# Optimization experiments

Hardware: AMD Instinct MI355X
Metric: run time of the kernel (lower is better)

The kernel has to match this reference:

```python
import jax, jax.numpy as jnp
import numpy as np

D = 512            # token_dim * num_heads
TOKEN_DIM = 256
SCALE = TOKEN_DIM ** (-0.5)
EPS = 1e-12        # torch F.normalize eps
FIDX = (0, 1, 1)   # original bug: out_rv uses final_myo


def l2norm(x, axis):
    n = jnp.sqrt(jnp.sum(x * x, axis=axis, keepdims=True))
    return x / jnp.maximum(n, EPS)


def setup_inputs() -> dict:
    key = jax.random.key(0)
    ks = jax.random.split(key, 16)
    B, N = 16, 1024
    s = 0.02
    return {
        "x_lv": jax.random.normal(ks[0], (B, N, D), jnp.float32),
        "x_myo": jax.random.normal(ks[1], (B, N, D), jnp.float32),
        "x_rv": jax.random.normal(ks[2], (B, N, D), jnp.float32),
        # stacked per-branch params: branch 0=lv, 1=myo, 2=rv
        "Wq": jax.random.normal(ks[3], (3, D, D), jnp.float32) * s,
        "bq": jax.random.normal(ks[4], (3, D), jnp.float32) * s,
        "Wk": jax.random.normal(ks[5], (3, D, D), jnp.float32) * s,
        "bk": jax.random.normal(ks[6], (3, D), jnp.float32) * s,
        "wg": jax.random.normal(ks[7], (3, D, 1), jnp.float32),
        "Wp": jax.random.normal(ks[8], (3, 3, D, D), jnp.float32) * s,  # [branch, key_src]
        "bp": jax.random.normal(ks[9], (3, 3, D), jnp.float32) * s,
        "Wf": jax.random.normal(ks[10], (3, D, TOKEN_DIM), jnp.float32) * s,
        "bf": jax.random.normal(ks[11], (3, TOKEN_DIM), jnp.float32) * s,
    }


def reference(x_lv, x_myo, x_rv, Wq, bq, Wk, bk, wg, Wp, bp, Wf, bf):
    X = (x_lv, x_myo, x_rv)
    # projections + L2 normalize over feature dim
    Q = [l2norm(X[m] @ Wq[m] + bq[m], axis=-1) for m in range(3)]  # [B,N,D]
    K = [l2norm(X[m] @ Wk[m] + bk[m], axis=-1) for m in range(3)]  # [B,N,D]
    outs = []
    for m in range(3):
        A = l2norm((Q[m] @ wg[m]) * SCALE, axis=1)       # [B,N,1], normed over seq
        G = jnp.sum(A * Q[m], axis=1)[:, None, :]        # [B,1,D] (broadcast repeat)
        acc = Q[m]
        for j in range(3):
            acc = acc + (G * K[j]) @ Wp[m, j] + bp[m, j]
        outs.append(acc @ Wf[FIDX[m]] + bf[FIDX[m]])     # [B,N,token_dim]
    return tuple(outs)
```

## Files before the change

kernel.cpp:

```cpp
#include <hip/hip_runtime.h>
#include <hip/hip_bf16.h>

typedef __hip_bfloat16 bf16;
typedef __attribute__((ext_vector_type(8))) short short8;
typedef __attribute__((ext_vector_type(4))) float f32x4;

#define SCALE_F 0.0625f

__device__ __forceinline__ float b2f(short s) {
  union { float f; unsigned int u; } x;
  x.u = ((unsigned int)(unsigned short)s) << 16;
  return x.f;
}
__device__ __forceinline__ unsigned short f2bu(float f) {
  __hip_bfloat16 h = __float2bfloat16(f);
  unsigned short u;
  __builtin_memcpy(&u, &h, 2);
  return u;
}
__device__ __forceinline__ void store_out(float* p, float v) { *p = v; }
__device__ __forceinline__ void store_out(bf16* p, float v) { *p = __float2bfloat16(v); }

typedef __attribute__((address_space(3))) void lds_void;
typedef __attribute__((address_space(1))) void gbl_void;

__device__ __forceinline__ void lds_load16(void* l, const void* g) {
  __builtin_amdgcn_global_load_lds((const gbl_void*)g, (lds_void*)l, 16, 0, 0);
}

template<typename OutT>
__device__ __forceinline__ void gemm_tile(
    const bf16* A0, const bf16* A1, const bf16* A2, const bf16* A3,
    int ldA, const bf16* Bt, int ldB, OutT* C, int ldC,
    const float* bias, int K, int row0, int col0)
{
  __shared__ bf16 As[128 * 32];
  __shared__ bf16 Bs[128 * 32];
  const int t = threadIdx.x;
  const int lane = t & 63;
  const int w = t >> 6;
  const int wm = w >> 1, wn = w & 1;
  const int lr = lane & 15, hi = lane >> 4;
  const int rA = t >> 2;
  const int kA = (t & 3) * 8;

  f32x4 acc[4][4];
#pragma unroll
  for (int i = 0; i < 4; ++i)
#pragma unroll
    for (int j = 0; j < 4; ++j) acc[i][j] = (f32x4){0.f, 0.f, 0.f, 0.f};

  const int nk = K >> 5;
  for (int kt = 0; kt < nk; ++kt) {
    const int k0 = kt << 5;
    const int s = k0 >> 9;
    const bf16* Aseg = (s == 0) ? A0 : (s == 1) ? A1 : (s == 2) ? A2 : A3;
    const int kl = (k0 & 511) + kA;
    __syncthreads();
    lds_load16(&As[t * 8],        Aseg + (size_t)(row0 + rA) * ldA + kl);
    lds_load16(&As[2048 + t * 8], Aseg + (size_t)(row0 + 64 + rA) * ldA + kl);
    lds_load16(&Bs[t * 8],        Bt + (size_t)(col0 + rA) * ldB + k0 + kA);
    lds_load16(&Bs[2048 + t * 8], Bt + (size_t)(col0 + 64 + rA) * ldB + k0 + kA);
    __syncthreads();
    short8 af[4], bfr[4];
#pragma unroll
    for (int f = 0; f < 4; ++f)
      af[f] = *(const short8*)&As[(wm * 64 + f * 16 + lr) * 32 + hi * 8];
#pragma unroll
    for (int f = 0; f < 4; ++f)
      bfr[f] = *(const short8*)&Bs[(wn * 64 + f * 16 + lr) * 32 + hi * 8];
#pragma unroll
    for (int i = 0; i < 4; ++i)
#pragma unroll
      for (int j = 0; j < 4; ++j)
        acc[i][j] = __builtin_amdgcn_mfma_f32_16x16x32_bf16(af[i], bfr[j], acc[i][j], 0, 0, 0);
  }

#pragma unroll
  for (int i = 0; i < 4; ++i) {
    const int rowb = row0 + wm * 64 + i * 16 + hi * 4;
#pragma unroll
    for (int j = 0; j < 4; ++j) {
      const int col = col0 + wn * 64 + j * 16 + lr;
      const float bv = bias ? bias[col] : 0.f;
      f32x4 v = acc[i][j];
#pragma unroll
      for (int r = 0; r < 4; ++r)
        store_out(&C[(size_t)(rowb + r) * ldC + col], v[r] + bv);
    }
  }
}

__global__ __launch_bounds__(256) void k_convert_x(
    const float* __restrict__ x0, const float* __restrict__ x1,
    const float* __restrict__ x2, bf16* __restrict__ xbf)
{
  const long long i = (long long)blockIdx.x * 256 + threadIdx.x;
  const int tt = (int)(i / 2097152);
  const long long e = i - (long long)tt * 2097152;
  const float4* src = (const float4*)(tt == 0 ? x0 : tt == 1 ? x1 : x2);
  float4 v = src[e];
  ushort4 o;
  o.x = f2bu(v.x); o.y = f2bu(v.y); o.z = f2bu(v.z); o.w = f2bu(v.w);
  ((ushort4*)xbf)[i] = o;
}

__global__ __launch_bounds__(256) void k_transpose(
    const float* __restrict__ in, bf16* __restrict__ out, int R, int C)
{
  const int tilesC = C >> 6;
  const int tr = (blockIdx.x / tilesC) << 6;
  const int tc = (blockIdx.x % tilesC) << 6;
  const size_t base = (size_t)blockIdx.y * R * C;
  __shared__ unsigned short tile[64][72];
  const int rr = threadIdx.x >> 4;
  const int cc = (threadIdx.x & 15) << 2;
#pragma unroll
  for (int p = 0; p < 4; ++p) {
    const int r = rr + (p << 4);
    float4 v = *(const float4*)&in[base + (size_t)(tr + r) * C + tc + cc];
    tile[cc + 0][r] = f2bu(v.x);
    tile[cc + 1][r] = f2bu(v.y);
    tile[cc + 2][r] = f2bu(v.z);
    tile[cc + 3][r] = f2bu(v.w);
  }
  __syncthreads();
#pragma unroll
  for (int p = 0; p < 4; ++p) {
    const int r = rr + (p << 4);
    ushort4 o;
    o.x = tile[r][cc + 0];
    o.y = tile[r][cc + 1];
    o.z = tile[r][cc + 2];
    o.w = tile[r][cc + 3];
    *(ushort4*)&out[base + (size_t)(tc + r) * R + tr + cc] = o;
  }
}

__global__ __launch_bounds__(256) void k_copy_bf16(
    const float* __restrict__ in, bf16* __restrict__ out)
{
  const long long i = (long long)blockIdx.x * 256 + threadIdx.x;
  float4 v = ((const float4*)in)[i];
  ushort4 o;
  o.x = f2bu(v.x); o.y = f2bu(v.y); o.z = f2bu(v.z); o.w = f2bu(v.w);
  ((ushort4*)out)[i] = o;
}

__global__ __launch_bounds__(256) void k_bprime(
    const float* __restrict__ bp, const float* __restrict__ Wf,
    const float* __restrict__ bfv, float* __restrict__ bpr)
{
  const int m = blockIdx.x;
  const int dc = blockIdx.y;
  const int n = threadIdx.x;
  const int fi = (m == 0) ? 0 : 1;
  float s = (dc == 0) ? bfv[fi * 256 + n] : 0.f;
  for (int d = dc * 64; d < dc * 64 + 64; ++d) {
    float b3 = bp[(m * 3 + 0) * 512 + d] + bp[(m * 3 + 1) * 512 + d] +
               bp[(m * 3 + 2) * 512 + d];
    s += b3 * Wf[(size_t)fi * 512 * 256 + (size_t)d * 256 + n];
  }
  atomicAdd(&bpr[m * 256 + n], s);
}

__global__ __launch_bounds__(256) void k_gemm1(
    const bf16* __restrict__ Xbf, const bf16* __restrict__ WT,
    const float* __restrict__ bq, const float* __restrict__ bk,
    bf16* __restrict__ QK)
{
  const int bid = blockIdx.x;
  const int swz = (bid & 7) * 384 + (bid >> 3);
  const int inst = swz >> 9;
  const int bx = swz & 511;
  const int m = (inst >= 3) ? inst - 3 : inst;
  const int tm = bx >> 2, tn = bx & 3;
  const bf16* A = Xbf + (size_t)m * (16384 * 512);
  const bf16* B = WT + (size_t)inst * (512 * 512);
  const float* bias = (inst < 3 ? bq : bk) + m * 512;
  bf16* C = QK + (size_t)inst * (16384 * 512);
  gemm_tile<bf16>(A, A, A, A, 512, B, 512, C, 512, bias, 512, tm * 128, tn * 128);
}

__global__ __launch_bounds__(256) void k_gemm_wpf(
    const bf16* __restrict__ WfT, const bf16* __restrict__ Wpbf,
    float* __restrict__ WpfT)
{
  const int inst = blockIdx.y;
  const int m = inst / 3;
  const int fi = (m == 0) ? 0 : 1;
  const int tm = blockIdx.x >> 2, tn = blockIdx.x & 3;
  const bf16* A = WfT + (size_t)fi * (256 * 512);
  const bf16* B = Wpbf + (size_t)inst * (512 * 512);
  float* C = WpfT + (size_t)inst * (256 * 512);
  gemm_tile<float>(A, A, A, A, 512, B, 512, C, 512, nullptr, 512, tm * 128, tn * 128);
}

__global__ __launch_bounds__(256) void k_gemm2(
    const bf16* __restrict__ QK, const bf16* __restrict__ W2T,
    const float* __restrict__ bpr, float* __restrict__ out)
{
  const int bid = blockIdx.x;
  const int swz = (bid & 7) * 96 + (bid >> 3);
  const int e = swz >> 4;
  const int bx = swz & 15;
  const int m = e >> 4, b = e & 15;
  const int tm = bx >> 1, tn = bx & 1;
  const bf16* A0 = QK + ((size_t)m * 16384 + (size_t)b * 1024) * 512;
  const bf16* A1 = QK + ((size_t)(3 * 16384) + (size_t)b * 1024) * 512;
  const bf16* A2 = QK + ((size_t)(4 * 16384) + (size_t)b * 1024) * 512;
  const bf16* A3 = QK + ((size_t)(5 * 16384) + (size_t)b * 1024) * 512;
  const bf16* Bt = W2T + (size_t)e * (256 * 2048);
  float* C = out + (size_t)e * (1024 * 256);
  gemm_tile<float>(A0, A1, A2, A3, 512, Bt, 2048, C, 256, bpr + m * 256, 2048,
                   tm * 128, tn * 128);
}

__global__ __launch_bounds__(256) void k_norm(
    bf16* __restrict__ QK, const float* __restrict__ wg, float* __restrict__ qdot)
{
  const int row = blockIdx.x * 4 + (threadIdx.x >> 6);
  const int lane = threadIdx.x & 63;
  bf16* p = QK + (size_t)row * 512 + lane * 8;
  short8 v = *(const short8*)p;
  float f[8];
  float ss = 0.f;
#pragma unroll
  for (int i = 0; i < 8; ++i) { f[i] = b2f(v[i]); ss += f[i] * f[i]; }
#pragma unroll
  for (int o = 32; o; o >>= 1) ss += __shfl_xor(ss, o);
  const float inv = 1.f / fmaxf(sqrtf(ss), 1e-12f);
  short8 ov;
#pragma unroll
  for (int i = 0; i < 8; ++i) ov[i] = (short)f2bu(f[i] * inv);
  *(short8*)p = ov;
  const int tt = row >> 14;
  if (tt < 3) {
    const float* wgm = wg + (size_t)tt * 512 + lane * 8;
    float dot = 0.f;
#pragma unroll
    for (int i = 0; i < 8; ++i) dot += f[i] * wgm[i];
    dot *= inv;
#pragma unroll
    for (int o = 32; o; o >>= 1) dot += __shfl_xor(dot, o);
    if (lane == 0) qdot[row] = dot;
  }
}

__global__ __launch_bounds__(256) void k_G(
    const float* __restrict__ qdot, const bf16* __restrict__ QK, float* __restrict__ G)
{
  const int e = blockIdx.x;
  const int m = e >> 4, b = e & 15;
  const int d0 = blockIdx.y << 6;
  __shared__ float Al[1024];
  __shared__ float red[4];
  __shared__ float Gp[4][64];
  const int t = threadIdx.x;
  const float* qd = qdot + (size_t)m * 16384 + (size_t)b * 1024;
  float ss = 0.f;
#pragma unroll
  for (int i = 0; i < 4; ++i) {
    float x = qd[t + i * 256] * SCALE_F;
    Al[t + i * 256] = x;
    ss += x * x;
  }
#pragma unroll
  for (int o = 32; o; o >>= 1) ss += __shfl_xor(ss, o);
  if ((t & 63) == 0) red[t >> 6] = ss;
  __syncthreads();
  const float inv = 1.f / fmaxf(sqrtf(red[0] + red[1] + red[2] + red[3]), 1e-12f);

  const int d = d0 + (t & 63);
  const int q = t >> 6;
  const bf16* Qb = QK + ((size_t)m * 16384 + (size_t)b * 1024) * 512 + d;
  float g = 0.f;
  for (int n = q * 256; n < q * 256 + 256; ++n)
    g += Al[n] * b2f(*(const short*)&Qb[(size_t)n * 512]);
  Gp[q][t & 63] = g;
  __syncthreads();
  if (t < 64)
    G[(size_t)e * 512 + d0 + t] = (Gp[0][t] + Gp[1][t] + Gp[2][t] + Gp[3][t]) * inv;
}

__global__ __launch_bounds__(256) void k_w2t(
    const bf16* __restrict__ WfT, const float* __restrict__ WpfT,
    const float* __restrict__ G, bf16* __restrict__ W2T)
{
  const int e = blockIdx.x;
  const int m = e >> 4;
  const int fi = (m == 0) ? 0 : 1;
  const int t = threadIdx.x;
  bf16* out = W2T + (size_t)e * (256 * 2048);
  __shared__ float Gl[512];
  Gl[t] = G[(size_t)e * 512 + t];
  Gl[t + 256] = G[(size_t)e * 512 + t + 256];
  __syncthreads();
  const int k = t * 8;
  for (int nr = 0; nr < 16; ++nr) {
    const int n = blockIdx.y * 16 + nr;
    if (k < 512) {
      *(short8*)&out[(size_t)n * 2048 + k] =
          *(const short8*)&WfT[((size_t)fi * 256 + n) * 512 + k];
    } else {
      const int j = (k >> 9) - 1;
      const int d = k & 511;
      const float* src = WpfT + (((size_t)(m * 3 + j) * 256 + n) * 512 + d);
      short8 o;
#pragma unroll
      for (int i = 0; i < 8; ++i) o[i] = (short)f2bu(Gl[d + i] * src[i]);
      *(short8*)&out[(size_t)n * 2048 + k] = o;
    }
  }
}

extern "C" void kernel_launch(void* const* d_in, const int* in_sizes, int n_in,
                              void* d_out, int out_size, void* d_ws, size_t ws_size,
                              hipStream_t stream) {
  const float* x_lv = (const float*)d_in[0];
  const float* x_myo = (const float*)d_in[1];
  const float* x_rv = (const float*)d_in[2];
  const float* Wq = (const float*)d_in[3];
  const float* bq = (const float*)d_in[4];
  const float* Wk = (const float*)d_in[5];
  const float* bk = (const float*)d_in[6];
  const float* wg = (const float*)d_in[7];
  const float* Wp = (const float*)d_in[8];
  const float* bp = (const float*)d_in[9];
  const float* Wf = (const float*)d_in[10];
  const float* bfv = (const float*)d_in[11];
  float* out = (float*)d_out;

  char* ws = (char*)d_ws;
  bf16* QK    = (bf16*)(ws);
  bf16* Xbf   = (bf16*)(ws + 100663296);
  bf16* WT    = (bf16*)(ws + 150994944);
  bf16* Wpbf  = (bf16*)(ws + 154140672);
  bf16* WfT   = (bf16*)(ws + 158859264);
  float* WpfT = (float*)(ws + 159383552);
  float* qdot = (float*)(ws + 164102144);
  float* G    = (float*)(ws + 164298752);
  float* bpr  = (float*)(ws + 164397056);
  bf16* W2T   = Xbf;

  k_convert_x<<<24576, 256, 0, stream>>>(x_lv, x_myo, x_rv, Xbf);
  k_transpose<<<dim3(64, 3), 256, 0, stream>>>(Wq, WT, 512, 512);
  k_transpose<<<dim3(64, 3), 256, 0, stream>>>(Wk, WT + 3 * 512 * 512, 512, 512);
  k_transpose<<<dim3(32, 2), 256, 0, stream>>>(Wf, WfT, 512, 256);
  k_copy_bf16<<<2304, 256, 0, stream>>>(Wp, Wpbf);
  hipMemsetAsync(bpr, 0, 3 * 256 * sizeof(float), stream);
  k_bprime<<<dim3(3, 8), 256, 0, stream>>>(bp, Wf, bfv, bpr);

  k_gemm1<<<3072, 256, 0, stream>>>(Xbf, WT, bq, bk, QK);

  k_norm<<<24576, 256, 0, stream>>>(QK, wg, qdot);

  k_gemm_wpf<<<dim3(8, 9), 256, 0, stream>>>(WfT, Wpbf, WpfT);

  k_G<<<dim3(48, 8), 256, 0, stream>>>(qdot, QK, G);

  k_w2t<<<dim3(48, 16), 256, 0, stream>>>(WfT, WpfT, G, W2T);

  k_gemm2<<<768, 256, 0, stream>>>(QK, W2T, bpr, out);
}
```

Before: 390.8 us.

## Use 256x256 double-buffered GEMM tile with 512 threads for main GEMMs

Adds a new GEMM tile routine computing 256x256 output tiles with 8 waves, K-step 64, double-buffered LDS staging via global_load_lds, XOR-swizzled LDS layout, and setprio around MFMA bursts. Both large GEMMs (QKV projection and final fused output GEMM) switch to it with new block swizzles so Q/K tiles sharing the same X rows are adjacent. This raises arithmetic intensity per block and overlaps loads with compute, at the cost of 128KB LDS per block, higher register pressure and far fewer blocks (192 for gemm2), which may underfill the 256 CUs.

```diff
diff --git a/kernel.cpp b/kernel.cpp
--- a/kernel.cpp
+++ b/kernel.cpp
@@ -26,6 +26,105 @@
 
 __device__ __forceinline__ void lds_load16(void* l, const void* g) {
   __builtin_amdgcn_global_load_lds((const gbl_void*)g, (lds_void*)l, 16, 0, 0);
+}
+
+template<typename OutT>
+__device__ __forceinline__ void gemm256_tile(
+    const bf16* A0, const bf16* A1, const bf16* A2, const bf16* A3, int ldA,
+    const bf16* Bt, int ldB, OutT* C, int ldC, const float* bias,
+    int K, int row0, int col0)
+{
+  __shared__ bf16 Abuf0[256 * 64], Abuf1[256 * 64];
+  __shared__ bf16 Bbuf0[256 * 64], Bbuf1[256 * 64];
+  const int tid = threadIdx.x;
+  const int lane = tid & 63, w = tid >> 6;
+  const int wm = w >> 2, wn = w & 3;
+  const int lr = lane & 15, hi = lane >> 4;
+
+  const int stageR = tid >> 3;
+  const int stageC = ((tid & 7) ^ (stageR & 7)) << 3;
+  const bf16* Bg0 = Bt + (size_t)(col0 + stageR) * ldB + stageC;
+
+  auto stage = [&](int bsel, int k0) {
+    const int seg = k0 >> 9;
+    const bf16* Aseg = (seg == 0) ? A0 : (seg == 1) ? A1 : (seg == 2) ? A2 : A3;
+    const bf16* Ag = Aseg + (size_t)(row0 + stageR) * ldA + (k0 & 511) + stageC;
+    const bf16* Bg = Bg0 + k0;
+    bf16* Al = (bsel ? Abuf1 : Abuf0) + tid * 8;
+    bf16* Bl = (bsel ? Bbuf1 : Bbuf0) + tid * 8;
+#pragma unroll
+    for (int q = 0; q < 4; ++q) {
+      lds_load16(Al + q * 4096, Ag + (size_t)q * 64 * ldA);
+      lds_load16(Bl + q * 4096, Bg + (size_t)q * 64 * ldB);
+    }
+  };
+
+  const int aoffb = (wm * 128 + lr) * 128;
+  const int boffb = (wn * 64 + lr) * 128;
+  const int s0 = ((hi ^ (lr & 7)) << 4);
+  const int s1 = (((4 + hi) ^ (lr & 7)) << 4);
+
+  f32x4 acc[8][4];
+#pragma unroll
+  for (int i = 0; i < 8; ++i)
+#pragma unroll
+    for (int j = 0; j < 4; ++j) acc[i][j] = (f32x4){0.f, 0.f, 0.f, 0.f};
+
+  const int nt = K >> 6;
+  stage(0, 0);
+  stage(1, 64);
+  asm volatile("s_waitcnt vmcnt(8)" ::: "memory");
+  __builtin_amdgcn_s_barrier();
+
+  for (int t = 0; t < nt; ++t) {
+    const char* Ab = (const char*)((t & 1) ? Abuf1 : Abuf0);
+    const char* Bb = (const char*)((t & 1) ? Bbuf1 : Bbuf0);
+    short8 ra[8], rb[4], ra2[8], rb2[4];
+#pragma unroll
+    for (int fr = 0; fr < 8; ++fr) ra[fr] = *(const short8*)(Ab + aoffb + fr * 2048 + s0);
+#pragma unroll
+    for (int fq = 0; fq < 4; ++fq) rb[fq] = *(const short8*)(Bb + boffb + fq * 2048 + s0);
+    __builtin_amdgcn_s_setprio(1);
+#pragma unroll
+    for (int fr = 0; fr < 8; ++fr)
+#pragma unroll
+      for (int fq = 0; fq < 4; ++fq)
+        acc[fr][fq] = __builtin_amdgcn_mfma_f32_16x16x32_bf16(ra[fr], rb[fq], acc[fr][fq], 0, 0, 0);
+    __builtin_amdgcn_s_setprio(0);
+#pragma unroll
+    for (int fr = 0; fr < 8; ++fr) ra2[fr] = *(const short8*)(Ab + aoffb + fr * 2048 + s1);
+#pragma unroll
+    for (int fq = 0; fq < 4; ++fq) rb2[fq] = *(const short8*)(Bb + boffb + fq * 2048 + s1);
+    asm volatile("s_waitcnt lgkmcnt(0)" ::: "memory");
+    __builtin_amdgcn_s_barrier();
+    if (t + 2 < nt) stage(t & 1, (t + 2) << 6);
+    __builtin_amdgcn_s_setprio(1);
+#pragma unroll
+    for (int fr = 0; fr < 8; ++fr)
+#pragma unroll
+      for (int fq = 0; fq < 4; ++fq)
+        acc[fr][fq] = __builtin_amdgcn_mfma_f32_16x16x32_bf16(ra2[fr], rb2[fq], acc[fr][fq], 0, 0, 0);
+    __builtin_amdgcn_s_setprio(0);
+    if (t + 1 < nt) {
+      if (t + 2 < nt) asm volatile("s_waitcnt vmcnt(8)" ::: "memory");
+      else            asm volatile("s_waitcnt vmcnt(0)" ::: "memory");
+      __builtin_amdgcn_s_barrier();
+    }
+  }
+
+#pragma unroll
+  for (int fr = 0; fr < 8; ++fr) {
+    const int rowb = row0 + wm * 128 + fr * 16 + hi * 4;
+#pragma unroll
+    for (int fq = 0; fq < 4; ++fq) {
+      const int col = col0 + wn * 64 + fq * 16 + lr;
+      const float bv = bias ? bias[col] : 0.f;
+      f32x4 v = acc[fr][fq];
+#pragma unroll
+      for (int r = 0; r < 4; ++r)
+        store_out(&C[(size_t)(rowb + r) * ldC + col], v[r] + bv);
+    }
+  }
 }
 
 template<typename OutT>
@@ -164,22 +263,24 @@
   atomicAdd(&bpr[m * 256 + n], s);
 }
 
-__global__ __launch_bounds__(256) void k_gemm1(
+__global__ __launch_bounds__(512, 2) void k_gemm1(
     const bf16* __restrict__ Xbf, const bf16* __restrict__ WT,
     const float* __restrict__ bq, const float* __restrict__ bk,
     bf16* __restrict__ QK)
 {
   const int bid = blockIdx.x;
-  const int swz = (bid & 7) * 384 + (bid >> 3);
-  const int inst = swz >> 9;
-  const int bx = swz & 511;
-  const int m = (inst >= 3) ? inst - 3 : inst;
-  const int tm = bx >> 2, tn = bx & 3;
+  const int swz = (bid & 7) * 96 + (bid >> 3);
+  const int m = swz >> 8;
+  const int rem = swz & 255;
+  const int tm = rem >> 2;
+  const int tn = (rem >> 1) & 1;
+  const int qk = rem & 1;
+  const int inst = qk ? (m + 3) : m;
   const bf16* A = Xbf + (size_t)m * (16384 * 512);
   const bf16* B = WT + (size_t)inst * (512 * 512);
-  const float* bias = (inst < 3 ? bq : bk) + m * 512;
+  const float* bias = (qk ? bk : bq) + m * 512;
   bf16* C = QK + (size_t)inst * (16384 * 512);
-  gemm_tile<bf16>(A, A, A, A, 512, B, 512, C, 512, bias, 512, tm * 128, tn * 128);
+  gemm256_tile<bf16>(A, A, A, A, 512, B, 512, C, 512, bias, 512, tm * 256, tn * 256);
 }
 
 __global__ __launch_bounds__(256) void k_gemm_wpf(
@@ -196,24 +297,25 @@
   gemm_tile<float>(A, A, A, A, 512, B, 512, C, 512, nullptr, 512, tm * 128, tn * 128);
 }
 
-__global__ __launch_bounds__(256) void k_gemm2(
+__global__ __launch_bounds__(512, 2) void k_gemm2(
     const bf16* __restrict__ QK, const bf16* __restrict__ W2T,
     const float* __restrict__ bpr, float* __restrict__ out)
 {
   const int bid = blockIdx.x;
-  const int swz = (bid & 7) * 96 + (bid >> 3);
-  const int e = swz >> 4;
-  const int bx = swz & 15;
-  const int m = e >> 4, b = e & 15;
-  const int tm = bx >> 1, tn = bx & 1;
+  const int swz = (bid & 7) * 24 + (bid >> 3);
+  const int b = swz / 12;
+  const int rem = swz % 12;
+  const int m = rem >> 2;
+  const int tm = rem & 3;
+  const int e = m * 16 + b;
   const bf16* A0 = QK + ((size_t)m * 16384 + (size_t)b * 1024) * 512;
   const bf16* A1 = QK + ((size_t)(3 * 16384) + (size_t)b * 1024) * 512;
   const bf16* A2 = QK + ((size_t)(4 * 16384) + (size_t)b * 1024) * 512;
   const bf16* A3 = QK + ((size_t)(5 * 16384) + (size_t)b * 1024) * 512;
   const bf16* Bt = W2T + (size_t)e * (256 * 2048);
   float* C = out + (size_t)e * (1024 * 256);
-  gemm_tile<float>(A0, A1, A2, A3, 512, Bt, 2048, C, 256, bpr + m * 256, 2048,
-                   tm * 128, tn * 128);
+  gemm256_tile<float>(A0, A1, A2, A3, 512, Bt, 2048, C, 256, bpr + m * 256, 2048,
+                      tm * 256, 0);
 }
 
 __global__ __launch_bounds__(256) void k_norm(
@@ -351,7 +453,7 @@
   hipMemsetAsync(bpr, 0, 3 * 256 * sizeof(float), stream);
   k_bprime<<<dim3(3, 8), 256, 0, stream>>>(bp, Wf, bfv, bpr);
 
-  k_gemm1<<<3072, 256, 0, stream>>>(Xbf, WT, bq, bk, QK);
+  k_gemm1<<<768, 512, 0, stream>>>(Xbf, WT, bq, bk, QK);
 
   k_norm<<<24576, 256, 0, stream>>>(QK, wg, qdot);
 
@@ -361,5 +463,5 @@
 
   k_w2t<<<dim3(48, 16), 256, 0, stream>>>(WfT, WpfT, G, W2T);
 
-  k_gemm2<<<768, 256, 0, stream>>>(QK, W2T, bpr, out);
-}
+  k_gemm2<<<192, 512, 0, stream>>>(QK, W2T, bpr, out);
+}
```

Measured after the change: 379.8 us. 2.8% less time.
